# Kernel tuning notes

Hardware: AMD Instinct MI355X
Metric: run time of the kernel (lower is better)

Reference implementation:

```python
import jax, jax.numpy as jnp
import numpy as np

N = 50000       # num nodes
F_IN = 256      # num_features
HID = 128       # num_hidden
E = 800000      # structural edges (no self loops)
E_KNN = 500000  # knn edges (no self loops)


def setup_inputs() -> dict:
    rng = np.random.default_rng(0)
    # loop-free random edges: col != row guaranteed
    row = rng.integers(0, N, E)
    col = (row + 1 + rng.integers(0, N - 1, E)) % N
    edge_index = jnp.asarray(np.stack([row, col]), dtype=jnp.int32)
    rowk = rng.integers(0, N, E_KNN)
    colk = (rowk + 1 + rng.integers(0, N - 1, E_KNN)) % N
    knn_graph = jnp.asarray(np.stack([rowk, colk]), dtype=jnp.int32)

    key = jax.random.key(0)
    ks = jax.random.split(key, 8)
    x = jax.random.normal(ks[0], (N, F_IN), dtype=jnp.float32)
    s = 1.0 / np.sqrt(F_IN)  # nn.Linear default init range
    def lin(kw, kb):
        W = jax.random.uniform(kw, (HID, F_IN), minval=-s, maxval=s, dtype=jnp.float32)
        b = jax.random.uniform(kb, (HID,), minval=-s, maxval=s, dtype=jnp.float32)
        return W, b
    W_s1, b_s1 = lin(ks[1], ks[2])
    W_s2, b_s2 = lin(ks[3], ks[4])
    W_f2, b_f2 = lin(ks[5], ks[6])
    return {"x": x, "edge_index": edge_index, "knn_graph": knn_graph,
            "W_s1": W_s1, "b_s1": b_s1, "W_s2": W_s2, "b_s2": b_s2,
            "W_f2": W_f2, "b_f2": b_f2}


def _gcn_norm(edge_index, num_nodes):
    # add_remaining_self_loops on loop-free input == append all self loops (w=1)
    loop = jnp.arange(num_nodes, dtype=edge_index.dtype)
    row = jnp.concatenate([edge_index[0], loop])
    col = jnp.concatenate([edge_index[1], loop])
    w = jnp.ones(row.shape[0], dtype=jnp.float32)
    deg = jax.ops.segment_sum(w, col, num_segments=num_nodes)
    dinv = jnp.where(deg > 0, jax.lax.rsqrt(deg), 0.0)
    return row, col, dinv[row] * w * dinv[col]


def _gcn(x, W, b, row, col, norm, K):
    # eval mode: dropout(p=0.6) is identity
    h = x @ W.T + b
    n = x.shape[0]
    for _ in range(K):
        # gather source feats -> edge-weight scale -> scatter-add to targets (SpMM)
        h = jax.ops.segment_sum(norm[:, None] * h[row], col, num_segments=n)
    return h


def reference(x, edge_index, knn_graph, W_s1, b_s1, W_s2, b_s2, W_f2, b_f2):
    n = x.shape[0]
    r, c, nm = _gcn_norm(edge_index, n)
    rk, ck, nmk = _gcn_norm(knn_graph, n)
    h0 = _gcn(x, W_s1, b_s1, r, c, nm, 2)
    h1 = _gcn(x, W_s2, b_s2, r, c, nm, 10)
    z0 = _gcn(x, W_f2, b_f2, r, c, nm, 2)
    # original computes gcn_f2(x, edge_index, K=2) twice; in eval mode both equal z0
    z1 = z0 + _gcn(x, W_f2, b_f2, rk, ck, nmk, 1)
    return (h0, h1, z0, z1)
```

## Files before the change

### kernel.cpp

```cpp
#include <hip/hip_runtime.h>
#include <hip/hip_fp16.h>

#define F_IN 256
#define HID 128

typedef _Float16 half8 __attribute__((ext_vector_type(8)));
typedef _Float16 half4v __attribute__((ext_vector_type(4)));
typedef float f32x4 __attribute__((ext_vector_type(4)));
typedef unsigned int uint4v __attribute__((ext_vector_type(4)));


__global__ void k_count2(const int* __restrict__ col_s, int E, int* __restrict__ cnt_s,
                         const int* __restrict__ col_k, int EK, int* __restrict__ cnt_k) {
  int e = blockIdx.x * blockDim.x + threadIdx.x;
  if (e < E) {
    atomicAdd(&cnt_s[col_s[e]], 1);
  } else {
    int f = e - E;
    if (f < EK) atomicAdd(&cnt_k[col_k[f]], 1);
  }
}

__global__ void k_scan_block(const int* __restrict__ in, int n, int* __restrict__ out,
                             int* __restrict__ bsum) {
  __shared__ int s[1024];
  int tid = threadIdx.x;
  int i = blockIdx.x * 1024 + tid;
  int v = (i < n) ? in[i] : 0;
  s[tid] = v;
  __syncthreads();
  for (int off = 1; off < 1024; off <<= 1) {
    int t = (tid >= off) ? s[tid - off] : 0;
    __syncthreads();
    s[tid] += t;
    __syncthreads();
  }
  if (i < n) out[i] = s[tid] - v;
  if (tid == 1023) bsum[blockIdx.x] = s[1023];
}

__global__ void k_scan_single(int* __restrict__ bsum, int nb, int* __restrict__ tail) {
  if (threadIdx.x == 0 && blockIdx.x == 0) {
    int run = 0;
    for (int b = 0; b < nb; ++b) { int t = bsum[b]; bsum[b] = run; run += t; }
    *tail = run;
  }
}

__global__ void k_add_off(int* __restrict__ out, const int* __restrict__ bsum, int n) {
  int i = blockIdx.x * blockDim.x + threadIdx.x;
  if (i < n) out[i] += bsum[i >> 10];
}

__global__ void k_scatter2(const int* __restrict__ row_s, const int* __restrict__ col_s, int E,
                           const int* __restrict__ offs_s, int* __restrict__ cur_s,
                           int* __restrict__ csr_s,
                           const int* __restrict__ row_k, const int* __restrict__ col_k, int EK,
                           const int* __restrict__ offs_k, int* __restrict__ cur_k,
                           int* __restrict__ csr_k) {
  int e = blockIdx.x * blockDim.x + threadIdx.x;
  if (e < E) {
    int c = col_s[e];
    int p = offs_s[c] + atomicAdd(&cur_s[c], 1);
    csr_s[p] = row_s[e];
  } else {
    int f = e - E;
    if (f < EK) {
      int c = col_k[f];
      int p = offs_k[c] + atomicAdd(&cur_k[c], 1);
      csr_k[p] = row_k[f];
    }
  }
}


__global__ void k_cvt_w(const float* __restrict__ W0, const float* __restrict__ W1,
                        const float* __restrict__ W2, _Float16* __restrict__ Wh) {
  const int sz = HID * F_IN;
  int idx = (blockIdx.x * 256 + threadIdx.x) * 4;
  const float* src = (idx < sz) ? (W0 + idx)
                   : (idx < 2 * sz) ? (W1 + idx - sz)
                   : (W2 + idx - 2 * sz);
  float4 v = *(const float4*)src;
  half4v o;
  o[0] = (_Float16)v.x; o[1] = (_Float16)v.y; o[2] = (_Float16)v.z; o[3] = (_Float16)v.w;
  *(half4v*)(Wh + idx) = o;
}


__global__ __launch_bounds__(256, 6) void k_gemm3(
    const float* __restrict__ x, const _Float16* __restrict__ Wh,
    const float* __restrict__ b0, const float* __restrict__ b1, const float* __restrict__ b2,
    int n, const int* __restrict__ cnt_s, const int* __restrict__ cnt_k,
    _Float16* __restrict__ gS1, _Float16* __restrict__ gS2,
    _Float16* __restrict__ gF2s, _Float16* __restrict__ gF2k)
{
  __shared__ _Float16 xs[32 * F_IN];
  int tid = threadIdx.x;
  int m0 = blockIdx.x * 32;

  {
    int r = tid >> 3;
    int cbase = (tid & 7) * 32;
    int gr = m0 + r; if (gr >= n) gr = n - 1;
    const float* src = x + (size_t)gr * F_IN + cbase;
    unsigned sw = (unsigned)((r & 7) << 4);
    char* drow = (char*)xs + r * (F_IN * 2);
#pragma unroll
    for (int i = 0; i < 4; ++i) {
      float4 a = *(const float4*)(src + i * 8);
      float4 b = *(const float4*)(src + i * 8 + 4);
      half8 v;
      v[0] = (_Float16)a.x; v[1] = (_Float16)a.y; v[2] = (_Float16)a.z; v[3] = (_Float16)a.w;
      v[4] = (_Float16)b.x; v[5] = (_Float16)b.y; v[6] = (_Float16)b.z; v[7] = (_Float16)b.w;
      *(half8*)(drow + (((unsigned)(cbase * 2 + i * 16)) ^ sw)) = v;
    }
  }
  __syncthreads();

  int lane = tid & 63;
  int wv = tid >> 6;
  int mh = wv >> 1, ch = wv & 1;
  int l15 = lane & 15, lhi = lane >> 4;
  int rloc = mh * 16 + l15;
  unsigned swr = (unsigned)((rloc & 7) << 4);
  const char* xrow = (const char*)xs + rloc * (F_IN * 2);

  int node = m0 + rloc;
  int cn = (node < n) ? node : (n - 1);
  float ss = rsqrtf((float)(cnt_s[cn] + 1));
  float sk = rsqrtf((float)(cnt_k[cn] + 1));

#pragma unroll 1
  for (int w = 0; w < 3; ++w) {
    const float* bias = (w == 0) ? b0 : (w == 1) ? b1 : b2;
    _Float16* dst = (w == 0) ? gS1 : (w == 1) ? gS2 : gF2s;
    const _Float16* Wp = Wh + (size_t)w * HID * F_IN
                            + (size_t)(ch * 64 + l15) * F_IN + lhi * 8;

    f32x4 acc[4];
#pragma unroll
    for (int nt = 0; nt < 4; ++nt) {
      float4 bv = *(const float4*)(bias + ch * 64 + nt * 16 + lhi * 4);
      acc[nt] = (f32x4){bv.x, bv.y, bv.z, bv.w};
    }

    half8 xf = *(const half8*)(xrow + (((unsigned)((0 * 32 + lhi * 8) * 2)) ^ swr));
    half8 wf[4];
#pragma unroll
    for (int nt = 0; nt < 4; ++nt)
      wf[nt] = *(const half8*)(Wp + (size_t)nt * 16 * F_IN + 0 * 32);

#pragma unroll
    for (int kt = 0; kt < 8; ++kt) {
      half8 xfn; half8 wfn[4];
      if (kt < 7) {
        xfn = *(const half8*)(xrow + (((unsigned)(((kt + 1) * 32 + lhi * 8) * 2)) ^ swr));
#pragma unroll
        for (int nt = 0; nt < 4; ++nt)
          wfn[nt] = *(const half8*)(Wp + (size_t)nt * 16 * F_IN + (kt + 1) * 32);
      }
#pragma unroll
      for (int nt = 0; nt < 4; ++nt)
        acc[nt] = __builtin_amdgcn_mfma_f32_16x16x32_f16(wf[nt], xf, acc[nt], 0, 0, 0);
      if (kt < 7) {
        xf = xfn;
#pragma unroll
        for (int nt = 0; nt < 4; ++nt) wf[nt] = wfn[nt];
      }
    }

    if (node < n) {
      size_t obase = (size_t)node * HID + ch * 64 + lhi * 4;
#pragma unroll
      for (int nt = 0; nt < 4; ++nt) {
        half4v o;
        o[0] = (_Float16)(acc[nt][0] * ss); o[1] = (_Float16)(acc[nt][1] * ss);
        o[2] = (_Float16)(acc[nt][2] * ss); o[3] = (_Float16)(acc[nt][3] * ss);
        *(half4v*)(dst + obase + nt * 16) = o;
      }
      if (w == 2) {
#pragma unroll
        for (int nt = 0; nt < 4; ++nt) {
          half4v o2;
          o2[0] = (_Float16)(acc[nt][0] * sk); o2[1] = (_Float16)(acc[nt][1] * sk);
          o2[2] = (_Float16)(acc[nt][2] * sk); o2[3] = (_Float16)(acc[nt][3] * sk);
          *(half4v*)(gF2k + obase + nt * 16) = o2;
        }
      }
    }
  }
}


__device__ inline float2 h2f2(unsigned int u) {
  __half2 h; *(unsigned int*)&h = u; return __half22float2(h);
}

__global__ __launch_bounds__(256) void k_spmm_h(
    const _Float16* __restrict__ gin, void* __restrict__ gout,
    const int* __restrict__ csr, const int* __restrict__ offs, const int* __restrict__ cnt,
    int n, int mode, const float* __restrict__ addsrc)
{
  int w = (blockIdx.x << 2) | ((int)threadIdx.x >> 6);
  if (w >= n) return;
  int lane = threadIdx.x & 63;
  int g = lane >> 4;
  int c = lane & 15;
  int beg = offs[w], end = offs[w + 1];

  float acc[8];
#pragma unroll
  for (int i = 0; i < 8; ++i) acc[i] = 0.f;

  int e = beg;
#pragma unroll 1
  for (; e + 16 <= end; e += 16) {
    int idx[4];
#pragma unroll
    for (int j = 0; j < 4; ++j) idx[j] = csr[e + 4 * j + g];
    uint4v u[4];
#pragma unroll
    for (int j = 0; j < 4; ++j)
      u[j] = *(const uint4v*)(gin + ((size_t)(unsigned)idx[j] << 7) + c * 8);
#pragma unroll
    for (int j = 0; j < 4; ++j)
#pragma unroll
      for (int q = 0; q < 4; ++q) {
        float2 v = h2f2(u[j][q]);
        acc[q * 2] += v.x; acc[q * 2 + 1] += v.y;
      }
  }
#pragma unroll 1
  for (; e + 4 <= end; e += 4) {
    int idx = csr[e + g];
    uint4v u = *(const uint4v*)(gin + ((size_t)(unsigned)idx << 7) + c * 8);
#pragma unroll
    for (int q = 0; q < 4; ++q) {
      float2 v = h2f2(u[q]);
      acc[q * 2] += v.x; acc[q * 2 + 1] += v.y;
    }
  }
  {
    int rem = end - e;
    if (g < rem) {
      int idx = csr[e + g];
      uint4v u = *(const uint4v*)(gin + ((size_t)(unsigned)idx << 7) + c * 8);
#pragma unroll
      for (int q = 0; q < 4; ++q) {
        float2 v = h2f2(u[q]);
        acc[q * 2] += v.x; acc[q * 2 + 1] += v.y;
      }
    }
  }
#pragma unroll
  for (int i = 0; i < 8; ++i) {
    acc[i] += __shfl_xor(acc[i], 16, 64);
    acc[i] += __shfl_xor(acc[i], 32, 64);
  }
  {
    uint4v u = *(const uint4v*)(gin + ((size_t)w << 7) + c * 8);
#pragma unroll
    for (int q = 0; q < 4; ++q) {
      float2 v = h2f2(u[q]);
      acc[q * 2] += v.x; acc[q * 2 + 1] += v.y;
    }
  }

  float deg = (float)(cnt[w] + 1);
  if (mode == 0) {
    float sc = 1.0f / deg;
    if (g == 0) {
      uint4v o;
#pragma unroll
      for (int q = 0; q < 4; ++q) {
        __half2 h = __float22half2_rn(make_float2(acc[q * 2] * sc, acc[q * 2 + 1] * sc));
        o[q] = *(unsigned int*)&h;
      }
      *(uint4v*)((_Float16*)gout + ((size_t)w << 7) + c * 8) = o;
    }
  } else {
    float sc = rsqrtf(deg);
    if (g == 0) {
      float o[8];
#pragma unroll
      for (int i = 0; i < 8; ++i) o[i] = acc[i] * sc;
      if (mode == 2) {
        const float* ap = addsrc + ((size_t)w << 7) + c * 8;
        float4 a0 = *(const float4*)ap;
        float4 a1 = *(const float4*)(ap + 4);
        o[0] += a0.x; o[1] += a0.y; o[2] += a0.z; o[3] += a0.w;
        o[4] += a1.x; o[5] += a1.y; o[6] += a1.z; o[7] += a1.w;
      }
      float* op = (float*)gout + ((size_t)w << 7) + c * 8;
      *(float4*)op = make_float4(o[0], o[1], o[2], o[3]);
      *(float4*)(op + 4) = make_float4(o[4], o[5], o[6], o[7]);
    }
  }
}

__global__ __launch_bounds__(256) void k_spmm3(
    const _Float16* __restrict__ g0, const _Float16* __restrict__ g1,
    const _Float16* __restrict__ g2,
    void* __restrict__ o0, void* __restrict__ o1, void* __restrict__ o2,
    int md0, int md1, int md2,
    const int* __restrict__ csr, const int* __restrict__ offs, const int* __restrict__ cnt,
    int n)
{
  int w = (blockIdx.x << 2) | ((int)threadIdx.x >> 6);
  if (w >= n) return;
  int lane = threadIdx.x & 63;
  int g = lane >> 4;
  int c = lane & 15;
  int beg = offs[w], end = offs[w + 1];

  float a0[8], a1[8], a2[8];
#pragma unroll
  for (int i = 0; i < 8; ++i) { a0[i] = 0.f; a1[i] = 0.f; a2[i] = 0.f; }

  int e = beg;
#pragma unroll 1
  for (; e + 4 <= end; e += 4) {
    size_t off = ((size_t)(unsigned)csr[e + g] << 7) + c * 8;
    uint4v u0 = *(const uint4v*)(g0 + off);
    uint4v u1 = *(const uint4v*)(g1 + off);
    uint4v u2 = *(const uint4v*)(g2 + off);
#pragma unroll
    for (int q = 0; q < 4; ++q) {
      float2 v;
      v = h2f2(u0[q]); a0[q * 2] += v.x; a0[q * 2 + 1] += v.y;
      v = h2f2(u1[q]); a1[q * 2] += v.x; a1[q * 2 + 1] += v.y;
      v = h2f2(u2[q]); a2[q * 2] += v.x; a2[q * 2 + 1] += v.y;
    }
  }
  {
    int rem = end - e;
    if (g < rem) {
      size_t off = ((size_t)(unsigned)csr[e + g] << 7) + c * 8;
      uint4v u0 = *(const uint4v*)(g0 + off);
      uint4v u1 = *(const uint4v*)(g1 + off);
      uint4v u2 = *(const uint4v*)(g2 + off);
#pragma unroll
      for (int q = 0; q < 4; ++q) {
        float2 v;
        v = h2f2(u0[q]); a0[q * 2] += v.x; a0[q * 2 + 1] += v.y;
        v = h2f2(u1[q]); a1[q * 2] += v.x; a1[q * 2 + 1] += v.y;
        v = h2f2(u2[q]); a2[q * 2] += v.x; a2[q * 2 + 1] += v.y;
      }
    }
  }
#pragma unroll
  for (int i = 0; i < 8; ++i) {
    a0[i] += __shfl_xor(a0[i], 16, 64); a0[i] += __shfl_xor(a0[i], 32, 64);
    a1[i] += __shfl_xor(a1[i], 16, 64); a1[i] += __shfl_xor(a1[i], 32, 64);
    a2[i] += __shfl_xor(a2[i], 16, 64); a2[i] += __shfl_xor(a2[i], 32, 64);
  }
  {
    size_t off = ((size_t)w << 7) + c * 8;
    uint4v u0 = *(const uint4v*)(g0 + off);
    uint4v u1 = *(const uint4v*)(g1 + off);
    uint4v u2 = *(const uint4v*)(g2 + off);
#pragma unroll
    for (int q = 0; q < 4; ++q) {
      float2 v;
      v = h2f2(u0[q]); a0[q * 2] += v.x; a0[q * 2 + 1] += v.y;
      v = h2f2(u1[q]); a1[q * 2] += v.x; a1[q * 2 + 1] += v.y;
      v = h2f2(u2[q]); a2[q * 2] += v.x; a2[q * 2 + 1] += v.y;
    }
  }

  float deg = (float)(cnt[w] + 1);
  if (g == 0) {
    float inv = 1.0f / deg, rs = rsqrtf(deg);
    {
      float sc = (md0 == 0) ? inv : rs;
      if (md0 == 0) {
        uint4v o;
#pragma unroll
        for (int q = 0; q < 4; ++q) {
          __half2 h = __float22half2_rn(make_float2(a0[q * 2] * sc, a0[q * 2 + 1] * sc));
          o[q] = *(unsigned int*)&h;
        }
        *(uint4v*)((_Float16*)o0 + ((size_t)w << 7) + c * 8) = o;
      } else {
        float* op = (float*)o0 + ((size_t)w << 7) + c * 8;
        *(float4*)op = make_float4(a0[0] * sc, a0[1] * sc, a0[2] * sc, a0[3] * sc);
        *(float4*)(op + 4) = make_float4(a0[4] * sc, a0[5] * sc, a0[6] * sc, a0[7] * sc);
      }
    }
    {
      float sc = (md1 == 0) ? inv : rs;
      if (md1 == 0) {
        uint4v o;
#pragma unroll
        for (int q = 0; q < 4; ++q) {
          __half2 h = __float22half2_rn(make_float2(a1[q * 2] * sc, a1[q * 2 + 1] * sc));
          o[q] = *(unsigned int*)&h;
        }
        *(uint4v*)((_Float16*)o1 + ((size_t)w << 7) + c * 8) = o;
      } else {
        float* op = (float*)o1 + ((size_t)w << 7) + c * 8;
        *(float4*)op = make_float4(a1[0] * sc, a1[1] * sc, a1[2] * sc, a1[3] * sc);
        *(float4*)(op + 4) = make_float4(a1[4] * sc, a1[5] * sc, a1[6] * sc, a1[7] * sc);
      }
    }
    {
      float sc = (md2 == 0) ? inv : rs;
      if (md2 == 0) {
        uint4v o;
#pragma unroll
        for (int q = 0; q < 4; ++q) {
          __half2 h = __float22half2_rn(make_float2(a2[q * 2] * sc, a2[q * 2 + 1] * sc));
          o[q] = *(unsigned int*)&h;
        }
        *(uint4v*)((_Float16*)o2 + ((size_t)w << 7) + c * 8) = o;
      } else {
        float* op = (float*)o2 + ((size_t)w << 7) + c * 8;
        *(float4*)op = make_float4(a2[0] * sc, a2[1] * sc, a2[2] * sc, a2[3] * sc);
        *(float4*)(op + 4) = make_float4(a2[4] * sc, a2[5] * sc, a2[6] * sc, a2[7] * sc);
      }
    }
  }
}


extern "C" void kernel_launch(void* const* d_in, const int* in_sizes, int n_in,
                              void* d_out, int out_size, void* d_ws, size_t ws_size,
                              hipStream_t stream) {
  const float* x    = (const float*)d_in[0];
  const int*   ei   = (const int*)d_in[1];
  const int*   knn  = (const int*)d_in[2];
  const float* W_s1 = (const float*)d_in[3];
  const float* b_s1 = (const float*)d_in[4];
  const float* W_s2 = (const float*)d_in[5];
  const float* b_s2 = (const float*)d_in[6];
  const float* W_f2 = (const float*)d_in[7];
  const float* b_f2 = (const float*)d_in[8];

  const int N  = in_sizes[0] / F_IN;
  const int E  = in_sizes[1] / 2;
  const int EK = in_sizes[2] / 2;
  const int* row_s = ei;   const int* col_s = ei + E;
  const int* row_k = knn;  const int* col_k = knn + EK;

  char* p = (char*)d_ws;
  auto carve = [&](size_t bytes) {
    char* r = p; p += (bytes + 511) & ~(size_t)511; return (void*)r;
  };
  int* cnt_s = (int*)carve((size_t)N * 4);
  int* cnt_k = (int*)carve((size_t)N * 4);
  int* cur_s = (int*)carve((size_t)N * 4);
  int* cur_k = (int*)carve((size_t)N * 4);
  char* zero_end = p;
  int* offs_s = (int*)carve((size_t)(N + 1) * 4);
  int* offs_k = (int*)carve((size_t)(N + 1) * 4);
  int* bsum   = (int*)carve(4096);
  int* csr_s  = (int*)carve((size_t)E * 4);
  int* csr_k  = (int*)carve((size_t)EK * 4);
  _Float16* Wh  = (_Float16*)carve((size_t)3 * HID * F_IN * 2);
  _Float16* gS1 = (_Float16*)carve((size_t)N * HID * 2);
  _Float16* gS2 = (_Float16*)carve((size_t)N * HID * 2);
  _Float16* gF2s= (_Float16*)carve((size_t)N * HID * 2);
  _Float16* gF2k= (_Float16*)carve((size_t)N * HID * 2);
  _Float16* tS2 = (_Float16*)carve((size_t)N * HID * 2);

  float* out_h0 = (float*)d_out;
  float* out_h1 = out_h0 + (size_t)N * HID;
  float* out_z0 = out_h1 + (size_t)N * HID;
  float* out_z1 = out_z0 + (size_t)N * HID;
  _Float16* tS1 = (_Float16*)out_z1;
  _Float16* tF2 = tS1 + (size_t)N * HID;

  hipMemsetAsync(d_ws, 0, (size_t)(zero_end - (char*)d_ws), stream);

  const int tpb = 256;
  int etot = E + EK;
  k_count2<<<(etot + tpb - 1) / tpb, tpb, 0, stream>>>(col_s, E, cnt_s, col_k, EK, cnt_k);

  int nb = (N + 1023) / 1024;
  k_scan_block<<<nb, 1024, 0, stream>>>(cnt_s, N, offs_s, bsum);
  k_scan_single<<<1, 64, 0, stream>>>(bsum, nb, offs_s + N);
  k_add_off<<<(N + tpb - 1) / tpb, tpb, 0, stream>>>(offs_s, bsum, N);
  k_scan_block<<<nb, 1024, 0, stream>>>(cnt_k, N, offs_k, bsum);
  k_scan_single<<<1, 64, 0, stream>>>(bsum, nb, offs_k + N);
  k_add_off<<<(N + tpb - 1) / tpb, tpb, 0, stream>>>(offs_k, bsum, N);

  k_scatter2<<<(etot + tpb - 1) / tpb, tpb, 0, stream>>>(
      row_s, col_s, E, offs_s, cur_s, csr_s,
      row_k, col_k, EK, offs_k, cur_k, csr_k);

  k_cvt_w<<<96, 256, 0, stream>>>(W_s1, W_s2, W_f2, Wh);
  k_gemm3<<<(N + 31) / 32, 256, 0, stream>>>(x, Wh, b_s1, b_s2, b_f2, N, cnt_s, cnt_k,
                                             gS1, gS2, gF2s, gF2k);

  int spmm_grid = (N + 3) / 4;

  k_spmm3<<<spmm_grid, 256, 0, stream>>>(gS1, gS2, gF2s,
                                         tS1, tS2, tF2, 0, 0, 0,
                                         csr_s, offs_s, cnt_s, N);
  k_spmm3<<<spmm_grid, 256, 0, stream>>>(tS1, tS2, tF2,
                                         out_h0, gS1, out_z0, 1, 0, 1,
                                         csr_s, offs_s, cnt_s, N);

  {
    _Float16* cur = gS1; _Float16* alt = tS2;
    for (int it = 0; it < 7; ++it) {
      k_spmm_h<<<spmm_grid, 256, 0, stream>>>(cur, alt,
                                              csr_s, offs_s, cnt_s, N, 0, nullptr);
      _Float16* t = cur; cur = alt; alt = t;
    }
    k_spmm_h<<<spmm_grid, 256, 0, stream>>>(cur, out_h1,
                                            csr_s, offs_s, cnt_s, N, 1, nullptr);
  }

  k_spmm_h<<<spmm_grid, 256, 0, stream>>>(gF2k, out_z1,
                                          csr_k, offs_k, cnt_k, N, 2,
                                          out_z0);
}
```

Measured before the change: 713.6 us.

## Retile projection GEMM to 64-row blocks with double-buffered LDS staging of x and W

The three-weight projection GEMM now uses 64-row tiles: each wave computes a 32x64 output sub-tile, and both the x tile and the fp16 weight tile go into double-buffered LDS, one K chunk of 64 at a time. Previously x was converted into LDS once and weights were read per wave straight from global memory. The aim is more MFMA work per LDS fragment and shared, coalesced weight loads across waves. In exchange, x is re-read from global for each of the three weight matrices, the kernel needs more LDS with a lower occupancy hint, and there is one barrier per K chunk.

```diff
diff --git a/kernel.cpp b/kernel.cpp
--- a/kernel.cpp
+++ b/kernel.cpp
@@ -88,104 +88,146 @@
 }
 
 
-__global__ __launch_bounds__(256, 6) void k_gemm3(
+__device__ inline half8 cvt8(float4 a, float4 b) {
+  half8 v;
+  v[0] = (_Float16)a.x; v[1] = (_Float16)a.y; v[2] = (_Float16)a.z; v[3] = (_Float16)a.w;
+  v[4] = (_Float16)b.x; v[5] = (_Float16)b.y; v[6] = (_Float16)b.z; v[7] = (_Float16)b.w;
+  return v;
+}
+
+__global__ __launch_bounds__(256, 3) void k_gemm3(
     const float* __restrict__ x, const _Float16* __restrict__ Wh,
     const float* __restrict__ b0, const float* __restrict__ b1, const float* __restrict__ b2,
     int n, const int* __restrict__ cnt_s, const int* __restrict__ cnt_k,
     _Float16* __restrict__ gS1, _Float16* __restrict__ gS2,
     _Float16* __restrict__ gF2s, _Float16* __restrict__ gF2k)
 {
-  __shared__ _Float16 xs[32 * F_IN];
+  __shared__ __align__(16) char lds[49152];
   int tid = threadIdx.x;
-  int m0 = blockIdx.x * 32;
-
-  {
-    int r = tid >> 3;
-    int cbase = (tid & 7) * 32;
-    int gr = m0 + r; if (gr >= n) gr = n - 1;
-    const float* src = x + (size_t)gr * F_IN + cbase;
-    unsigned sw = (unsigned)((r & 7) << 4);
-    char* drow = (char*)xs + r * (F_IN * 2);
-#pragma unroll
-    for (int i = 0; i < 4; ++i) {
-      float4 a = *(const float4*)(src + i * 8);
-      float4 b = *(const float4*)(src + i * 8 + 4);
-      half8 v;
-      v[0] = (_Float16)a.x; v[1] = (_Float16)a.y; v[2] = (_Float16)a.z; v[3] = (_Float16)a.w;
-      v[4] = (_Float16)b.x; v[5] = (_Float16)b.y; v[6] = (_Float16)b.z; v[7] = (_Float16)b.w;
-      *(half8*)(drow + (((unsigned)(cbase * 2 + i * 16)) ^ sw)) = v;
-    }
-  }
-  __syncthreads();
+  int m0 = blockIdx.x * 64;
+
+  int rA = tid >> 2;
+  int cA0 = (tid & 3) * 2, cA1 = cA0 + 1;
+  int gnA = m0 + rA; if (gnA >= n) gnA = n - 1;
+  const float* xA = x + (size_t)gnA * F_IN;
+  unsigned aw0 = (unsigned)(rA * 128 + ((cA0 ^ (rA & 7)) << 4));
+  unsigned aw1 = (unsigned)(rA * 128 + ((cA1 ^ (rA & 7)) << 4));
+  int rB = tid >> 1;
+  int cB0 = (tid & 1) * 4;
+  unsigned bw[4];
+#pragma unroll
+  for (int i = 0; i < 4; ++i)
+    bw[i] = (unsigned)(rB * 128 + (((cB0 + i) ^ (rB & 7)) << 4));
 
   int lane = tid & 63;
   int wv = tid >> 6;
-  int mh = wv >> 1, ch = wv & 1;
+  int wm = wv >> 1, wn = wv & 1;
   int l15 = lane & 15, lhi = lane >> 4;
-  int rloc = mh * 16 + l15;
-  unsigned swr = (unsigned)((rloc & 7) << 4);
-  const char* xrow = (const char*)xs + rloc * (F_IN * 2);
-
-  int node = m0 + rloc;
-  int cn = (node < n) ? node : (n - 1);
-  float ss = rsqrtf((float)(cnt_s[cn] + 1));
-  float sk = rsqrtf((float)(cnt_k[cn] + 1));
+  unsigned koff0 = (unsigned)(((0 * 4 + lhi) ^ (l15 & 7)) << 4);
+  unsigned koff1 = (unsigned)(((1 * 4 + lhi) ^ (l15 & 7)) << 4);
+  unsigned raw0 = (unsigned)((wm * 32 + 0 * 16 + l15) * 128);
+  unsigned raw1 = (unsigned)((wm * 32 + 1 * 16 + l15) * 128);
+  unsigned rbw[4];
+#pragma unroll
+  for (int ni = 0; ni < 4; ++ni)
+    rbw[ni] = (unsigned)((wn * 64 + ni * 16 + l15) * 128);
+
+  int nodebase = m0 + wm * 32 + l15;
+  float ss[2], sk[2];
+#pragma unroll
+  for (int mi = 0; mi < 2; ++mi) {
+    int nd = nodebase + mi * 16;
+    int cn = (nd < n) ? nd : (n - 1);
+    ss[mi] = rsqrtf((float)(cnt_s[cn] + 1));
+    sk[mi] = rsqrtf((float)(cnt_k[cn] + 1));
+  }
 
 #pragma unroll 1
   for (int w = 0; w < 3; ++w) {
     const float* bias = (w == 0) ? b0 : (w == 1) ? b1 : b2;
     _Float16* dst = (w == 0) ? gS1 : (w == 1) ? gS2 : gF2s;
-    const _Float16* Wp = Wh + (size_t)w * HID * F_IN
-                            + (size_t)(ch * 64 + l15) * F_IN + lhi * 8;
-
-    f32x4 acc[4];
-#pragma unroll
-    for (int nt = 0; nt < 4; ++nt) {
-      float4 bv = *(const float4*)(bias + ch * 64 + nt * 16 + lhi * 4);
-      acc[nt] = (f32x4){bv.x, bv.y, bv.z, bv.w};
-    }
-
-    half8 xf = *(const half8*)(xrow + (((unsigned)((0 * 32 + lhi * 8) * 2)) ^ swr));
-    half8 wf[4];
-#pragma unroll
-    for (int nt = 0; nt < 4; ++nt)
-      wf[nt] = *(const half8*)(Wp + (size_t)nt * 16 * F_IN + 0 * 32);
-
-#pragma unroll
-    for (int kt = 0; kt < 8; ++kt) {
-      half8 xfn; half8 wfn[4];
-      if (kt < 7) {
-        xfn = *(const half8*)(xrow + (((unsigned)(((kt + 1) * 32 + lhi * 8) * 2)) ^ swr));
-#pragma unroll
-        for (int nt = 0; nt < 4; ++nt)
-          wfn[nt] = *(const half8*)(Wp + (size_t)nt * 16 * F_IN + (kt + 1) * 32);
-      }
-#pragma unroll
-      for (int nt = 0; nt < 4; ++nt)
-        acc[nt] = __builtin_amdgcn_mfma_f32_16x16x32_f16(wf[nt], xf, acc[nt], 0, 0, 0);
-      if (kt < 7) {
-        xf = xfn;
-#pragma unroll
-        for (int nt = 0; nt < 4; ++nt) wf[nt] = wfn[nt];
-      }
-    }
-
-    if (node < n) {
-      size_t obase = (size_t)node * HID + ch * 64 + lhi * 4;
-#pragma unroll
-      for (int nt = 0; nt < 4; ++nt) {
-        half4v o;
-        o[0] = (_Float16)(acc[nt][0] * ss); o[1] = (_Float16)(acc[nt][1] * ss);
-        o[2] = (_Float16)(acc[nt][2] * ss); o[3] = (_Float16)(acc[nt][3] * ss);
-        *(half4v*)(dst + obase + nt * 16) = o;
-      }
-      if (w == 2) {
-#pragma unroll
-        for (int nt = 0; nt < 4; ++nt) {
-          half4v o2;
-          o2[0] = (_Float16)(acc[nt][0] * sk); o2[1] = (_Float16)(acc[nt][1] * sk);
-          o2[2] = (_Float16)(acc[nt][2] * sk); o2[3] = (_Float16)(acc[nt][3] * sk);
-          *(half4v*)(gF2k + obase + nt * 16) = o2;
+    const _Float16* WB = Wh + (size_t)w * (HID * F_IN) + (size_t)rB * F_IN;
+
+    f32x4 acc[2][4];
+#pragma unroll
+    for (int ni = 0; ni < 4; ++ni) {
+      float4 bv = *(const float4*)(bias + wn * 64 + ni * 16 + lhi * 4);
+      f32x4 b4 = {bv.x, bv.y, bv.z, bv.w};
+      acc[0][ni] = b4; acc[1][ni] = b4;
+    }
+
+    float4 fa[4]; uint4v ub[4];
+    fa[0] = *(const float4*)(xA + 0 * 64 + cA0 * 8);
+    fa[1] = *(const float4*)(xA + 0 * 64 + cA0 * 8 + 4);
+    fa[2] = *(const float4*)(xA + 0 * 64 + cA1 * 8);
+    fa[3] = *(const float4*)(xA + 0 * 64 + cA1 * 8 + 4);
+#pragma unroll
+    for (int i = 0; i < 4; ++i)
+      ub[i] = *(const uint4v*)(WB + 0 * 64 + (cB0 + i) * 8);
+
+#pragma unroll
+    for (int kt = 0; kt < 4; ++kt) {
+      char* Ab = lds + (kt & 1) * 8192;
+      char* Bb = lds + 16384 + (kt & 1) * 16384;
+      *(half8*)(Ab + aw0) = cvt8(fa[0], fa[1]);
+      *(half8*)(Ab + aw1) = cvt8(fa[2], fa[3]);
+#pragma unroll
+      for (int i = 0; i < 4; ++i) *(uint4v*)(Bb + bw[i]) = ub[i];
+      if (kt < 3) {
+        fa[0] = *(const float4*)(xA + (kt + 1) * 64 + cA0 * 8);
+        fa[1] = *(const float4*)(xA + (kt + 1) * 64 + cA0 * 8 + 4);
+        fa[2] = *(const float4*)(xA + (kt + 1) * 64 + cA1 * 8);
+        fa[3] = *(const float4*)(xA + (kt + 1) * 64 + cA1 * 8 + 4);
+#pragma unroll
+        for (int i = 0; i < 4; ++i)
+          ub[i] = *(const uint4v*)(WB + (kt + 1) * 64 + (cB0 + i) * 8);
+      }
+      __syncthreads();
+      {
+        const char* Ar = Ab; const char* Br = Bb;
+#pragma unroll
+        for (int ks = 0; ks < 2; ++ks) {
+          unsigned ko = ks ? koff1 : koff0;
+          half8 xf0 = *(const half8*)(Ar + raw0 + ko);
+          half8 xf1 = *(const half8*)(Ar + raw1 + ko);
+          half8 wf0 = *(const half8*)(Br + rbw[0] + ko);
+          half8 wf1 = *(const half8*)(Br + rbw[1] + ko);
+          half8 wf2 = *(const half8*)(Br + rbw[2] + ko);
+          half8 wf3 = *(const half8*)(Br + rbw[3] + ko);
+          acc[0][0] = __builtin_amdgcn_mfma_f32_16x16x32_f16(wf0, xf0, acc[0][0], 0, 0, 0);
+          acc[0][1] = __builtin_amdgcn_mfma_f32_16x16x32_f16(wf1, xf0, acc[0][1], 0, 0, 0);
+          acc[0][2] = __builtin_amdgcn_mfma_f32_16x16x32_f16(wf2, xf0, acc[0][2], 0, 0, 0);
+          acc[0][3] = __builtin_amdgcn_mfma_f32_16x16x32_f16(wf3, xf0, acc[0][3], 0, 0, 0);
+          acc[1][0] = __builtin_amdgcn_mfma_f32_16x16x32_f16(wf0, xf1, acc[1][0], 0, 0, 0);
+          acc[1][1] = __builtin_amdgcn_mfma_f32_16x16x32_f16(wf1, xf1, acc[1][1], 0, 0, 0);
+          acc[1][2] = __builtin_amdgcn_mfma_f32_16x16x32_f16(wf2, xf1, acc[1][2], 0, 0, 0);
+          acc[1][3] = __builtin_amdgcn_mfma_f32_16x16x32_f16(wf3, xf1, acc[1][3], 0, 0, 0);
+        }
+      }
+    }
+
+#pragma unroll
+    for (int mi = 0; mi < 2; ++mi) {
+      int nd = nodebase + mi * 16;
+      if (nd < n) {
+        size_t ob = (size_t)nd * HID + wn * 64 + lhi * 4;
+        float s1 = ss[mi];
+#pragma unroll
+        for (int ni = 0; ni < 4; ++ni) {
+          half4v o;
+          o[0] = (_Float16)(acc[mi][ni][0] * s1); o[1] = (_Float16)(acc[mi][ni][1] * s1);
+          o[2] = (_Float16)(acc[mi][ni][2] * s1); o[3] = (_Float16)(acc[mi][ni][3] * s1);
+          *(half4v*)(dst + ob + ni * 16) = o;
+        }
+        if (w == 2) {
+          float s2 = sk[mi];
+#pragma unroll
+          for (int ni = 0; ni < 4; ++ni) {
+            half4v o2;
+            o2[0] = (_Float16)(acc[mi][ni][0] * s2); o2[1] = (_Float16)(acc[mi][ni][1] * s2);
+            o2[2] = (_Float16)(acc[mi][ni][2] * s2); o2[3] = (_Float16)(acc[mi][ni][3] * s2);
+            *(half4v*)(gF2k + ob + ni * 16) = o2;
+          }
         }
       }
     }
@@ -490,7 +532,7 @@
       row_k, col_k, EK, offs_k, cur_k, csr_k);
 
   k_cvt_w<<<96, 256, 0, stream>>>(W_s1, W_s2, W_f2, Wh);
-  k_gemm3<<<(N + 31) / 32, 256, 0, stream>>>(x, Wh, b_s1, b_s2, b_f2, N, cnt_s, cnt_k,
+  k_gemm3<<<(N + 63) / 64, 256, 0, stream>>>(x, Wh, b_s1, b_s2, b_f2, N, cnt_s, cnt_k,
                                              gS1, gS2, gF2s, gF2k);
 
   int spmm_grid = (N + 3) / 4;
```

Measured after the change: 658.4 us. -7.7%, faster.
